# Kernel optimization log

Hardware: AMD Instinct MI355X
Metric: run time of the kernel (lower is better)

The kernel has to match this reference:

```python
import jax, jax.numpy as jnp
import numpy as np

N_NODES = 100000
N_EDGES = 1600000
D_IN, D_HID, D_OUT = 256, 512, 48
K_STEPS = 10
ALPHA = 0.1


def setup_inputs() -> dict:
    key = jax.random.key(0)
    k_x, k_e, k_w1, k_w2 = jax.random.split(key, 4)
    x = jax.random.normal(k_x, (N_NODES, D_IN), dtype=jnp.float32)
    edge_index = jax.random.randint(k_e, (2, N_EDGES), 0, N_NODES, dtype=jnp.int64)
    # MLP params (Kaiming-ish scaling)
    W1 = jax.random.normal(k_w1, (D_IN, D_HID), dtype=jnp.float32) * (1.0 / np.sqrt(D_IN))
    b1 = jnp.zeros((D_HID,), dtype=jnp.float32)
    W2 = jax.random.normal(k_w2, (D_HID, D_OUT), dtype=jnp.float32) * (1.0 / np.sqrt(D_HID))
    b2 = jnp.zeros((D_OUT,), dtype=jnp.float32)
    return {"x": x, "edge_index": edge_index, "W1": W1, "b1": b1, "W2": W2, "b2": b2}


def reference(x, edge_index, W1, b1, W2, b2):
    N = x.shape[0]
    # --- MLP encoder ---
    h = jax.nn.relu(x @ W1 + b1) @ W2 + b2  # [N, D_OUT]

    # --- APPNP propagation (PyG defaults: add self-loops, symmetric gcn_norm) ---
    loop = jnp.arange(N, dtype=edge_index.dtype)
    src = jnp.concatenate([edge_index[0], loop])  # [E+N]
    dst = jnp.concatenate([edge_index[1], loop])
    ones = jnp.ones(src.shape[0], dtype=h.dtype)
    deg = jax.ops.segment_sum(ones, dst, num_segments=N)  # in-degree incl. self-loop
    dinv = jnp.where(deg > 0, jax.lax.rsqrt(deg), 0.0)
    norm = dinv[src] * dinv[dst]  # [E+N]

    out = h
    for _ in range(K_STEPS):
        msg = out[src] * norm[:, None]                      # gather + scale
        agg = jax.ops.segment_sum(msg, dst, num_segments=N)  # scatter-add
        out = (1.0 - ALPHA) * agg + ALPHA * h                # teleport mix
    return out
```

## Files before the change

### kernel.cpp

```cpp
#include <hip/hip_runtime.h>
#include <hip/hip_fp16.h>

constexpr int D_IN = 256, D_HID = 512, D_OUT = 48;
constexpr int HPAD = 64;
constexpr int K_STEPS = 10;
constexpr int CAPR = 96;

typedef __attribute__((ext_vector_type(8))) __bf16 bf16x8;
typedef __attribute__((ext_vector_type(4))) float f32x4;

__device__ __forceinline__ unsigned short f2bf(float f) {
  unsigned u = __builtin_bit_cast(unsigned, f);
  u += 0x7fffu + ((u >> 16) & 1u);
  return (unsigned short)(u >> 16);
}

__device__ __forceinline__ void gl2lds16(const unsigned short* g, unsigned short* l) {
  __builtin_amdgcn_global_load_lds(
      (const __attribute__((address_space(1))) unsigned int*)g,
      (__attribute__((address_space(3))) unsigned int*)l, 16, 0, 0);
}


__global__ void zero1_kernel(int* __restrict__ a, int N) {
  int i = blockIdx.x * 256 + threadIdx.x;
  if (i < N) a[i] = 0;
}

__global__ __launch_bounds__(256) void countfill_kernel(
    const int* __restrict__ src, const int* __restrict__ dst,
    int* __restrict__ cnt, int* __restrict__ edges, int E) {
  int e = blockIdx.x * 256 + threadIdx.x;
  if (e >= E) return;
  int d = __builtin_nontemporal_load(dst + e);
  int s = __builtin_nontemporal_load(src + e);
  int r = atomicAdd(&cnt[d], 1);
  edges[d * CAPR + r] = s;
}

__global__ void dinvdeg_kernel(const int* __restrict__ cnt, float* __restrict__ dinv,
                               int* __restrict__ pdeg, int N) {
  int n = blockIdx.x * 256 + threadIdx.x;
  if (n < N) {
    int c = cnt[n];
    dinv[n] = rsqrtf((float)(c + 1));
    pdeg[n] = (c + 4) & ~3;
  }
}

__global__ void pad_kernel(const int* __restrict__ cnt, const int* __restrict__ pdeg,
                           int* __restrict__ edges, int N) {
  int n = blockIdx.x * 256 + threadIdx.x;
  if (n >= N) return;
  int a = n * CAPR + cnt[n];
  int b = n * CAPR + pdeg[n];
  edges[a] = n;
  for (int p = a + 1; p < b; ++p) edges[p] = N;
}

__global__ void zrow_kernel(__half* __restrict__ a, __half* __restrict__ b, int N) {
  int t = threadIdx.x;
  a[(size_t)N * HPAD + t] = __float2half(0.f);
  b[(size_t)N * HPAD + t] = __float2half(0.f);
}


__global__ void convert_w1(const float* __restrict__ W1, unsigned short* __restrict__ W1F) {
  int i = blockIdx.x * 256 + threadIdx.x;
  if (i >= D_HID * D_IN) return;
  int c = i >> 8, k = i & 255;
  int ct = c >> 6, tn = (c >> 4) & 3, l15 = c & 15;
  int kb = k >> 5, q = (k >> 3) & 3, j = k & 7;
  int lane = (q << 4) | l15;
  int dst = (((ct * 4 + tn) * 8 + kb) << 9) + lane * 8 + j;
  W1F[dst] = f2bf(W1[k * D_HID + c]);
}

__global__ void convert_w2(const float* __restrict__ W2, unsigned short* __restrict__ W2F) {
  int i = blockIdx.x * 256 + threadIdx.x;
  if (i >= D_OUT * D_HID) return;
  int n = i >> 9, k = i & 511;
  int ct = k >> 6, kk = (k >> 5) & 1, q = (k >> 3) & 3, j = k & 7;
  int tn = n >> 4, l15 = n & 15;
  int lane = (q << 4) | l15;
  int dst = (((ct * 2 + kk) * 3 + tn) << 9) + lane * 8 + j;
  W2F[dst] = f2bf(W2[k * D_OUT + n]);
}


__global__ __launch_bounds__(512, 2) void encoder_kernel(
    const float* __restrict__ x, const float* __restrict__ b1,
    const float* __restrict__ b2, const float* __restrict__ dinvp,
    const unsigned short* __restrict__ W1F,
    const unsigned short* __restrict__ W2F,
    __half* __restrict__ h2, __half* __restrict__ qb, int N) {
  __shared__ unsigned short sW1[16384];
  __shared__ unsigned short sHid[8][16][72];
  __shared__ float sB1[512];
  __shared__ float sB2[64];

  int tid = threadIdx.x;
  int w = tid >> 6, lane = tid & 63;
  int q = lane >> 4, l15 = lane & 15;
  int row0 = blockIdx.x * 128 + w * 16;

  {
    const unsigned short* gsrc = W1F + (w << 9) + lane * 8;
    unsigned short* ldst = &sW1[w << 9];
#pragma unroll
    for (int i = 0; i < 4; ++i)
      gl2lds16(gsrc + (i << 12), ldst + (i << 12));
  }
  sB1[tid] = b1[tid];
  if (tid < 48) sB2[tid] = b2[tid];

  int grow = row0 + l15;
  bool rok = grow < N;
  const float* xr = x + (size_t)grow * D_IN;
  float4 xv[16];
#pragma unroll
  for (int jb = 0; jb < 8; ++jb) {
    xv[2 * jb]     = rok ? *(const float4*)(xr + jb * 32 + q * 8)
                         : make_float4(0.f, 0.f, 0.f, 0.f);
    xv[2 * jb + 1] = rok ? *(const float4*)(xr + jb * 32 + q * 8 + 4)
                         : make_float4(0.f, 0.f, 0.f, 0.f);
  }
  uint4 axu[8];
#pragma unroll
  for (int jb = 0; jb < 8; ++jb) {
    union { uint4 u; unsigned short s[8]; } uu;
    float4 v0 = xv[2 * jb], v1 = xv[2 * jb + 1];
    uu.s[0] = f2bf(v0.x); uu.s[1] = f2bf(v0.y); uu.s[2] = f2bf(v0.z); uu.s[3] = f2bf(v0.w);
    uu.s[4] = f2bf(v1.x); uu.s[5] = f2bf(v1.y); uu.s[6] = f2bf(v1.z); uu.s[7] = f2bf(v1.w);
    axu[jb] = uu.u;
  }

  f32x4 hacc[3];
#pragma unroll
  for (int t = 0; t < 3; ++t)
#pragma unroll
    for (int r = 0; r < 4; ++r) hacc[t][r] = 0.f;

  __syncthreads();

  for (int ct = 0; ct < 8; ++ct) {
    int c0 = ct * 64;
    f32x4 acc[4];
#pragma unroll
    for (int t = 0; t < 4; ++t)
#pragma unroll
      for (int r = 0; r < 4; ++r) acc[t][r] = 0.f;

    const unsigned short* sb = &sW1[lane * 8];
#pragma unroll
    for (int kb = 0; kb < 8; ++kb) {
      bf16x8 a = __builtin_bit_cast(bf16x8, axu[kb]);
      bf16x8 bq0 = *(const bf16x8*)(sb + (kb << 9));
      bf16x8 bq1 = *(const bf16x8*)(sb + (kb << 9) + 4096);
      bf16x8 bq2 = *(const bf16x8*)(sb + (kb << 9) + 8192);
      bf16x8 bq3 = *(const bf16x8*)(sb + (kb << 9) + 12288);
      acc[0] = __builtin_amdgcn_mfma_f32_16x16x32_bf16(a, bq0, acc[0], 0, 0, 0);
      acc[1] = __builtin_amdgcn_mfma_f32_16x16x32_bf16(a, bq1, acc[1], 0, 0, 0);
      acc[2] = __builtin_amdgcn_mfma_f32_16x16x32_bf16(a, bq2, acc[2], 0, 0, 0);
      acc[3] = __builtin_amdgcn_mfma_f32_16x16x32_bf16(a, bq3, acc[3], 0, 0, 0);
    }
#pragma unroll
    for (int tn = 0; tn < 4; ++tn) {
      int c = tn * 16 + l15;
      float bias = sB1[c0 + c];
#pragma unroll
      for (int rg = 0; rg < 4; ++rg) {
        float v = acc[tn][rg] + bias;
        v = v > 0.f ? v : 0.f;
        sHid[w][q * 4 + rg][c] = f2bf(v);
      }
    }
#pragma unroll
    for (int kk = 0; kk < 2; ++kk) {
      bf16x8 a0 = *(const bf16x8*)&sHid[w][l15][kk * 32 + q * 8];
      const unsigned short* w2b = W2F + (((ct * 2 + kk) * 3) << 9) + lane * 8;
#pragma unroll
      for (int tn = 0; tn < 3; ++tn) {
        bf16x8 b = *(const bf16x8*)(w2b + (tn << 9));
        hacc[tn] = __builtin_amdgcn_mfma_f32_16x16x32_bf16(a0, b, hacc[tn], 0, 0, 0);
      }
    }
    __syncthreads();
    if (ct < 7) {
      const unsigned short* gsrc = W1F + ((size_t)(ct + 1) << 14) + (w << 9) + lane * 8;
      unsigned short* ldst = &sW1[w << 9];
#pragma unroll
      for (int i = 0; i < 4; ++i)
        gl2lds16(gsrc + (i << 12), ldst + (i << 12));
      __syncthreads();
    }
  }
  float dv[4];
#pragma unroll
  for (int rg = 0; rg < 4; ++rg) {
    int gr = row0 + q * 4 + rg;
    dv[rg] = (gr < N) ? dinvp[gr] : 0.f;
  }
#pragma unroll
  for (int tn = 0; tn < 3; ++tn) {
    int c = tn * 16 + l15;
    float bias = sB2[c];
#pragma unroll
    for (int rg = 0; rg < 4; ++rg) {
      int gr = row0 + q * 4 + rg;
      if (gr < N) {
        float val = hacc[tn][rg] + bias;
        h2[(size_t)gr * HPAD + c] = __float2half(val);
        qb[(size_t)gr * HPAD + c] = __float2half(dv[rg] * val);
      }
    }
  }
#pragma unroll
  for (int rg = 0; rg < 4; ++rg) {
    int gr = row0 + q * 4 + rg;
    if (gr < N) {
      h2[(size_t)gr * HPAD + 48 + l15] = __float2half(0.f);
      qb[(size_t)gr * HPAD + 48 + l15] = __float2half(0.f);
    }
  }
}


__global__ __launch_bounds__(256) void prop_kernel(
    const __half* __restrict__ cur, const __half* __restrict__ h2,
    const float* __restrict__ dinv, const int* __restrict__ pdeg,
    const int* __restrict__ edges, __half* __restrict__ nxt,
    float* __restrict__ outf, int N, int last) {
  int wid = (blockIdx.x * 256 + threadIdx.x) >> 6;
  int lane = threadIdx.x & 63;
  int half = lane >> 5;
  int slot = (lane >> 3) & 3;
  int s = lane & 7;
  int node = wid * 2 + half;
  bool nok = node < N;
  int p0 = 0, p1 = 0;
  if (nok) { p0 = node * CAPR; p1 = p0 + pdeg[node]; }
  int d = p1 - p0;
  int dmax = max(d, __shfl_xor(d, 32));
  int nb = dmax >> 2;

  float acc[8];
#pragma unroll
  for (int i = 0; i < 8; ++i) acc[i] = 0.f;

  int p = p0 + slot;
  int e0 = N, e1 = N, e2 = N, e3 = N;
  if (nb > 0) e0 = edges[p];
  if (nb > 1) e1 = edges[p + 4];
  if (nb > 2) e2 = edges[p + 8];
  if (nb > 3) e3 = edges[p + 12];
  int b = 0;
  for (; b + 4 <= nb; b += 4) {
    int n0 = N, n1 = N, n2 = N, n3 = N;
    if (b + 4 < nb) n0 = edges[p + 16];
    if (b + 5 < nb) n1 = edges[p + 20];
    if (b + 6 < nb) n2 = edges[p + 24];
    if (b + 7 < nb) n3 = edges[p + 28];
    int i0 = (p      < p1) ? e0 : N;
    int i1 = (p + 4  < p1) ? e1 : N;
    int i2 = (p + 8  < p1) ? e2 : N;
    int i3 = (p + 12 < p1) ? e3 : N;
    union { float4 f; __half2 h[4]; } u0, u1, u2, u3;
    u0.f = *(const float4*)(cur + ((size_t)i0 << 6) + s * 8);
    u1.f = *(const float4*)(cur + ((size_t)i1 << 6) + s * 8);
    u2.f = *(const float4*)(cur + ((size_t)i2 << 6) + s * 8);
    u3.f = *(const float4*)(cur + ((size_t)i3 << 6) + s * 8);
#pragma unroll
    for (int i = 0; i < 4; ++i) {
      float2 f0 = __half22float2(u0.h[i]);
      float2 f1 = __half22float2(u1.h[i]);
      float2 f2 = __half22float2(u2.h[i]);
      float2 f3 = __half22float2(u3.h[i]);
      acc[2 * i]     += (f0.x + f1.x) + (f2.x + f3.x);
      acc[2 * i + 1] += (f0.y + f1.y) + (f2.y + f3.y);
    }
    e0 = n0; e1 = n1; e2 = n2; e3 = n3; p += 16;
  }
  if (b < nb) {
    int i0 = (p < p1) ? e0 : N;
    union { float4 f; __half2 h[4]; } u0;
    u0.f = *(const float4*)(cur + ((size_t)i0 << 6) + s * 8);
#pragma unroll
    for (int i = 0; i < 4; ++i) {
      float2 f0 = __half22float2(u0.h[i]);
      acc[2 * i]     += f0.x;
      acc[2 * i + 1] += f0.y;
    }
  }
  if (b + 1 < nb) {
    int i1 = (p + 4 < p1) ? e1 : N;
    union { float4 f; __half2 h[4]; } u1;
    u1.f = *(const float4*)(cur + ((size_t)i1 << 6) + s * 8);
#pragma unroll
    for (int i = 0; i < 4; ++i) {
      float2 f1 = __half22float2(u1.h[i]);
      acc[2 * i]     += f1.x;
      acc[2 * i + 1] += f1.y;
    }
  }
  if (b + 2 < nb) {
    int i2 = (p + 8 < p1) ? e2 : N;
    union { float4 f; __half2 h[4]; } u2;
    u2.f = *(const float4*)(cur + ((size_t)i2 << 6) + s * 8);
#pragma unroll
    for (int i = 0; i < 4; ++i) {
      float2 f2 = __half22float2(u2.h[i]);
      acc[2 * i]     += f2.x;
      acc[2 * i + 1] += f2.y;
    }
  }
#pragma unroll
  for (int i = 0; i < 8; ++i) {
    acc[i] += __int_as_float(__builtin_amdgcn_ds_swizzle(__float_as_int(acc[i]), 0x201F));
    acc[i] += __int_as_float(__builtin_amdgcn_ds_swizzle(__float_as_int(acc[i]), 0x401F));
  }
  if ((lane & 24) != 0 || !nok) return;
  float di = dinv[node];
  size_t base = ((size_t)node << 6) + s * 8;
  union { float4 f; __half2 h[4]; } uh;
  uh.f = *(const float4*)(h2 + base);
  float outv[8];
#pragma unroll
  for (int i = 0; i < 4; ++i) {
    float2 hf = __half22float2(uh.h[i]);
    outv[2 * i]     = 0.9f * di * acc[2 * i]     + 0.1f * hf.x;
    outv[2 * i + 1] = 0.9f * di * acc[2 * i + 1] + 0.1f * hf.y;
  }
  if (last) {
    if (s < 6) {
      float* op = outf + (size_t)node * D_OUT + s * 8;
      *(float4*)op       = make_float4(outv[0], outv[1], outv[2], outv[3]);
      *(float4*)(op + 4) = make_float4(outv[4], outv[5], outv[6], outv[7]);
    }
  } else {
    union { uint4 u4; __half2 h[4]; } o;
#pragma unroll
    for (int i = 0; i < 4; ++i)
      o.h[i] = __floats2half2_rn(di * outv[2 * i], di * outv[2 * i + 1]);
    *(uint4*)(nxt + base) = o.u4;
  }
}


extern "C" void kernel_launch(void* const* d_in, const int* in_sizes, int n_in,
                              void* d_out, int out_size, void* d_ws, size_t ws_size,
                              hipStream_t stream) {
  (void)n_in; (void)out_size; (void)ws_size;
  const float* x  = (const float*)d_in[0];
  const int*   ei = (const int*)d_in[1];
  const float* W1 = (const float*)d_in[2];
  const float* b1 = (const float*)d_in[3];
  const float* W2 = (const float*)d_in[4];
  const float* b2 = (const float*)d_in[5];
  const int N = in_sizes[0] / D_IN;
  const int E = in_sizes[1] / 2;
  const int* e_src = ei;
  const int* e_dst = ei + E;

  char* ws = (char*)d_ws;
  size_t off = 0;
  auto take = [&](size_t bytes) -> char* {
    char* p = ws + off;
    off += (bytes + 511) & ~(size_t)511;
    return p;
  };
  int* cnt      = (int*)take((size_t)N * 4);
  float* dinv   = (float*)take((size_t)N * 4);
  int* pdeg     = (int*)take((size_t)N * 4);
  int* edges    = (int*)take((size_t)N * CAPR * 4 + 1024);
  unsigned short* W1F = (unsigned short*)take((size_t)D_IN * D_HID * 2);
  unsigned short* W2F = (unsigned short*)take((size_t)D_HID * D_OUT * 2);
  __half* h2    = (__half*)take((size_t)N * HPAD * 2);
  __half* bufA  = (__half*)take((size_t)(N + 1) * HPAD * 2);
  __half* bufB  = (__half*)d_out;
  float* outp   = (float*)d_out;

  int nb256 = (N + 255) / 256;
  int eb256 = (E + 255) / 256;

  zero1_kernel<<<nb256, 256, 0, stream>>>(cnt, N);
  countfill_kernel<<<eb256, 256, 0, stream>>>(e_src, e_dst, cnt, edges, E);
  dinvdeg_kernel<<<nb256, 256, 0, stream>>>(cnt, dinv, pdeg, N);
  pad_kernel<<<nb256, 256, 0, stream>>>(cnt, pdeg, edges, N);
  zrow_kernel<<<1, 64, 0, stream>>>(bufA, bufB, N);

  convert_w1<<<(D_IN * D_HID + 255) / 256, 256, 0, stream>>>(W1, W1F);
  convert_w2<<<(D_HID * D_OUT + 255) / 256, 256, 0, stream>>>(W2, W2F);
  encoder_kernel<<<(N + 127) / 128, 512, 0, stream>>>(x, b1, b2, dinv, W1F, W2F,
                                                      h2, bufB, N);

  int waves = (N + 1) / 2;
  int pblocks = (waves + 3) / 4;
  const __half* src = bufB;
  __half* dst = bufA;
  for (int it = 1; it <= K_STEPS; ++it) {
    int last = (it == K_STEPS);
    prop_kernel<<<pblocks, 256, 0, stream>>>(src, h2, dinv, pdeg, edges,
                                             dst, outp, N, last);
    src = dst;
    dst = (dst == bufA) ? bufB : bufA;
  }
}
```

Before: 648.0 us.

## Bucket edges by destination range before CSR fill; double-buffer W1 staging

Result: faster. 625.4 us (-3.5%).

```diff
diff --git a/kernel.cpp b/kernel.cpp
--- a/kernel.cpp
+++ b/kernel.cpp
@@ -4,7 +4,8 @@
 constexpr int D_IN = 256, D_HID = 512, D_OUT = 48;
 constexpr int HPAD = 64;
 constexpr int K_STEPS = 10;
-constexpr int CAPR = 96;
+constexpr int CAPR = 64;
+constexpr int EB   = 4096;
 
 typedef __attribute__((ext_vector_type(8))) __bf16 bf16x8;
 typedef __attribute__((ext_vector_type(4))) float f32x4;
@@ -22,20 +23,57 @@
 }
 
 
-__global__ void zero1_kernel(int* __restrict__ a, int N) {
+__global__ void zero_kernel(int* __restrict__ cnt, int* __restrict__ gcur, int N) {
   int i = blockIdx.x * 256 + threadIdx.x;
-  if (i < N) a[i] = 0;
-}
-
-__global__ __launch_bounds__(256) void countfill_kernel(
+  if (i < N) cnt[i] = 0;
+  if (blockIdx.x == 0 && threadIdx.x < 256) gcur[threadIdx.x] = 0;
+}
+
+__global__ __launch_bounds__(256) void bucket_kernel(
     const int* __restrict__ src, const int* __restrict__ dst,
-    int* __restrict__ cnt, int* __restrict__ edges, int E) {
-  int e = blockIdx.x * 256 + threadIdx.x;
-  if (e >= E) return;
-  int d = __builtin_nontemporal_load(dst + e);
-  int s = __builtin_nontemporal_load(src + e);
-  int r = atomicAdd(&cnt[d], 1);
-  edges[d * CAPR + r] = s;
+    int2* __restrict__ fifo, int* __restrict__ gcur, int FCAP, int E) {
+  __shared__ int bcnt[256], bbase[256], brank[256];
+  int tid = threadIdx.x;
+  int e0 = blockIdx.x * EB;
+  bcnt[tid] = 0;
+  __syncthreads();
+  int sv[16], dv[16];
+#pragma unroll
+  for (int k = 0; k < 16; ++k) {
+    int e = e0 + k * 256 + tid;
+    if (e < E) {
+      dv[k] = __builtin_nontemporal_load(dst + e);
+      sv[k] = __builtin_nontemporal_load(src + e);
+      atomicAdd(&bcnt[dv[k] >> 9], 1);
+    } else {
+      dv[k] = -1;
+    }
+  }
+  __syncthreads();
+  if (bcnt[tid] > 0) bbase[tid] = atomicAdd(&gcur[tid], bcnt[tid]);
+  brank[tid] = 0;
+  __syncthreads();
+#pragma unroll
+  for (int k = 0; k < 16; ++k) {
+    if (dv[k] >= 0) {
+      int b = dv[k] >> 9;
+      int r = atomicAdd(&brank[b], 1);
+      fifo[(size_t)b * FCAP + bbase[b] + r] = make_int2(sv[k], dv[k]);
+    }
+  }
+}
+
+__global__ __launch_bounds__(256) void csr_kernel(
+    const int2* __restrict__ fifo, const int* __restrict__ gcur,
+    int* __restrict__ cnt, int* __restrict__ edges, int FCAP) {
+  int b = blockIdx.x;
+  int n = gcur[b];
+  const int2* f = fifo + (size_t)b * FCAP;
+  for (int i = threadIdx.x; i < n; i += 256) {
+    int2 v = f[i];
+    int r = atomicAdd(&cnt[v.y], 1);
+    edges[(size_t)v.y * CAPR + r] = v.x;
+  }
 }
 
 __global__ void dinvdeg_kernel(const int* __restrict__ cnt, float* __restrict__ dinv,
@@ -94,7 +132,7 @@
     const unsigned short* __restrict__ W1F,
     const unsigned short* __restrict__ W2F,
     __half* __restrict__ h2, __half* __restrict__ qb, int N) {
-  __shared__ unsigned short sW1[16384];
+  __shared__ unsigned short sW1[2][16384];
   __shared__ unsigned short sHid[8][16][72];
   __shared__ float sB1[512];
   __shared__ float sB2[64];
@@ -104,13 +142,15 @@
   int q = lane >> 4, l15 = lane & 15;
   int row0 = blockIdx.x * 128 + w * 16;
 
-  {
-    const unsigned short* gsrc = W1F + (w << 9) + lane * 8;
-    unsigned short* ldst = &sW1[w << 9];
+  auto stageCt = [&](int c, int half) {
+    const unsigned short* gsrc = W1F + ((size_t)c << 14) + (w << 9) + lane * 8;
+    unsigned short* ldst = &sW1[half][w << 9];
 #pragma unroll
     for (int i = 0; i < 4; ++i)
       gl2lds16(gsrc + (i << 12), ldst + (i << 12));
-  }
+  };
+
+  stageCt(0, 0);
   sB1[tid] = b1[tid];
   if (tid < 48) sB2[tid] = b2[tid];
 
@@ -144,6 +184,9 @@
   __syncthreads();
 
   for (int ct = 0; ct < 8; ++ct) {
+    int cur = ct & 1;
+    if (ct < 7) stageCt(ct + 1, cur ^ 1);
+
     int c0 = ct * 64;
     f32x4 acc[4];
 #pragma unroll
@@ -151,7 +194,7 @@
 #pragma unroll
       for (int r = 0; r < 4; ++r) acc[t][r] = 0.f;
 
-    const unsigned short* sb = &sW1[lane * 8];
+    const unsigned short* sb = &sW1[cur][lane * 8];
 #pragma unroll
     for (int kb = 0; kb < 8; ++kb) {
       bf16x8 a = __builtin_bit_cast(bf16x8, axu[kb]);
@@ -186,14 +229,6 @@
       }
     }
     __syncthreads();
-    if (ct < 7) {
-      const unsigned short* gsrc = W1F + ((size_t)(ct + 1) << 14) + (w << 9) + lane * 8;
-      unsigned short* ldst = &sW1[w << 9];
-#pragma unroll
-      for (int i = 0; i < 4; ++i)
-        gl2lds16(gsrc + (i << 12), ldst + (i << 12));
-      __syncthreads();
-    }
   }
   float dv[4];
 #pragma unroll
@@ -369,9 +404,13 @@
     off += (bytes + 511) & ~(size_t)511;
     return p;
   };
+  const int NB2  = (N + 511) >> 9;
+  const int FCAP = E / NB2 + 1024;
   int* cnt      = (int*)take((size_t)N * 4);
   float* dinv   = (float*)take((size_t)N * 4);
   int* pdeg     = (int*)take((size_t)N * 4);
+  int* gcur     = (int*)take(1024);
+  int2* fifo    = (int2*)take((size_t)NB2 * FCAP * 8);
   int* edges    = (int*)take((size_t)N * CAPR * 4 + 1024);
   unsigned short* W1F = (unsigned short*)take((size_t)D_IN * D_HID * 2);
   unsigned short* W2F = (unsigned short*)take((size_t)D_HID * D_OUT * 2);
@@ -381,10 +420,11 @@
   float* outp   = (float*)d_out;
 
   int nb256 = (N + 255) / 256;
-  int eb256 = (E + 255) / 256;
-
-  zero1_kernel<<<nb256, 256, 0, stream>>>(cnt, N);
-  countfill_kernel<<<eb256, 256, 0, stream>>>(e_src, e_dst, cnt, edges, E);
+  int ebB   = (E + EB - 1) / EB;
+
+  zero_kernel<<<nb256, 256, 0, stream>>>(cnt, gcur, N);
+  bucket_kernel<<<ebB, 256, 0, stream>>>(e_src, e_dst, fifo, gcur, FCAP, E);
+  csr_kernel<<<NB2, 256, 0, stream>>>(fifo, gcur, cnt, edges, FCAP);
   dinvdeg_kernel<<<nb256, 256, 0, stream>>>(cnt, dinv, pdeg, N);
   pad_kernel<<<nb256, 256, 0, stream>>>(cnt, pdeg, edges, N);
   zrow_kernel<<<1, 64, 0, stream>>>(bufA, bufB, N);
```
